# Kernel optimization log

Hardware: AMD Instinct MI355X
Metric: run time of the kernel (lower is better)

The kernel has to match this reference:

```python
import jax, jax.numpy as jnp
import numpy as np
import math

H, W = 32, 32
HID = 256
K = 4
B = 16
DIN = 272
DFF = 1024
L = 2
NB = 7
IMG_H, IMG_W = 256, 256
LN_EPS = 1e-5


def _layernorm(x, g, b):
    m = jnp.mean(x, axis=-1, keepdims=True)
    v = jnp.var(x, axis=-1, keepdims=True)
    return (x - m) / jnp.sqrt(v + LN_EPS) * g + b


def _neighbor_mask(h, w, nb):
    # (h*w, h*w): 0 inside the nb x nb window around each query pixel, -inf outside
    rr = jnp.repeat(jnp.arange(h), w)
    cc = jnp.tile(jnp.arange(w), h)
    near = (jnp.abs(rr[:, None] - rr[None, :]) <= nb // 2) & (
        jnp.abs(cc[:, None] - cc[None, :]) <= nb // 2
    )
    return jnp.where(near, 0.0, -jnp.inf).astype(jnp.float32)


def _pos_embed(row_embed, col_embed):
    # pos[i*w + j] = concat(col_embed[j], row_embed[i])  -> (h*w, hid)
    h, nf = row_embed.shape
    w = col_embed.shape[0]
    pe = jnp.concatenate(
        [
            jnp.broadcast_to(col_embed[None, :, :], (h, w, nf)),
            jnp.broadcast_to(row_embed[:, None, :], (h, w, nf)),
        ],
        axis=-1,
    )
    return pe.reshape(h * w, 2 * nf)


def _resize_bilinear_ac(x, oh, ow):
    # nn.UpsamplingBilinear2d => align_corners=True
    b, c, h, w = x.shape
    ys = jnp.arange(oh) * ((h - 1) / (oh - 1))
    y0 = jnp.floor(ys).astype(jnp.int32)
    y1 = jnp.minimum(y0 + 1, h - 1)
    fy = (ys - y0).astype(x.dtype)
    x = x[:, :, y0, :] * (1 - fy)[None, None, :, None] + x[:, :, y1, :] * fy[None, None, :, None]
    xs = jnp.arange(ow) * ((w - 1) / (ow - 1))
    x0 = jnp.floor(xs).astype(jnp.int32)
    x1 = jnp.minimum(x0 + 1, w - 1)
    fx = (xs - x0).astype(x.dtype)
    x = x[:, :, :, x0] * (1 - fx) + x[:, :, :, x1] * fx
    return x


def _forward(query_features, matched_features, qW, qb, kvW, kvb, row_embed, col_embed,
             aggW, aggb, n1g, n1b, l1W, l1b, l2W, l2b, n2g, n2b, outW, outb):
    b, c_in, h, w = query_features.shape
    n = h * w
    # b c h w -> b (h w) c, then input projections
    qt = query_features.transpose(0, 2, 3, 1).reshape(b, n, c_in) @ qW + qb  # (b,n,hid)
    kt = matched_features.transpose(0, 1, 3, 4, 2).reshape(K, b, n, c_in) @ kvW + kvb  # (K,b,n,hid)

    pos = _pos_embed(row_embed, col_embed)  # (n, hid); broadcast over batch
    mask = _neighbor_mask(h, w, NB)  # (n, n)
    scale = 1.0 / math.sqrt(qt.shape[-1])

    x = qt
    for l in range(L):
        qp = (x + pos) * scale            # q gets pos embed then scaled
        kp = kt + pos                     # k gets pos embed; v is the raw matched tokens
        scores = jnp.einsum('bnc,kbmc->kbnm', qp, kp) + mask
        attn = jax.nn.softmax(scores, axis=-1)
        o = jnp.einsum('kbnm,kbmc->bnkc', attn, kt).reshape(b, n, K * HID)
        o = o @ aggW[l] + aggb[l]
        x = _layernorm(x + o, n1g[l], n1b[l])
        ff = jax.nn.relu(x @ l1W[l] + l1b[l]) @ l2W[l] + l2b[l]
        x = _layernorm(x + ff, n2g[l], n2b[l])

    recon_tokens = x @ outW + outb  # (b,n,c_in)
    recon = recon_tokens.reshape(b, h, w, c_in).transpose(0, 3, 1, 2)
    pred = jnp.sqrt(jnp.sum((recon - query_features) ** 2, axis=1, keepdims=True))
    pred = (pred - pred.min()) / (pred.max() - pred.min())
    pred = _resize_bilinear_ac(pred, IMG_H, IMG_W)
    return recon, pred


def setup_inputs() -> dict:
    key = jax.random.key(0)
    ks = jax.random.split(key, 12)

    def nrm(k, shape, scale=0.02):
        return jax.random.normal(k, shape, jnp.float32) * scale

    return {
        'query_features': jax.random.normal(ks[0], (B, DIN, H, W), jnp.float32),
        'matched_features': jax.random.normal(ks[1], (K, B, DIN, H, W), jnp.float32),
        'qW': nrm(ks[2], (DIN, HID)), 'qb': jnp.zeros((HID,), jnp.float32),
        'kvW': nrm(ks[3], (DIN, HID)), 'kvb': jnp.zeros((HID,), jnp.float32),
        'row_embed': jax.random.uniform(ks[4], (H, HID // 2), jnp.float32),
        'col_embed': jax.random.uniform(ks[5], (W, HID // 2), jnp.float32),
        'aggW': nrm(ks[6], (L, K * HID, HID)), 'aggb': jnp.zeros((L, HID), jnp.float32),
        'n1g': jnp.ones((L, HID), jnp.float32), 'n1b': jnp.zeros((L, HID), jnp.float32),
        'l1W': nrm(ks[7], (L, HID, DFF)), 'l1b': jnp.zeros((L, DFF), jnp.float32),
        'l2W': nrm(ks[8], (L, DFF, HID)), 'l2b': jnp.zeros((L, HID), jnp.float32),
        'n2g': jnp.ones((L, HID), jnp.float32), 'n2b': jnp.zeros((L, HID), jnp.float32),
        'outW': nrm(ks[9], (HID, DIN)), 'outb': jnp.zeros((DIN,), jnp.float32),
    }


def reference(query_features, matched_features, qW, qb, kvW, kvb, row_embed, col_embed,
              aggW, aggb, n1g, n1b, l1W, l1b, l2W, l2b, n2g, n2b, outW, outb):
    return _forward(query_features, matched_features, qW, qb, kvW, kvb, row_embed,
                    col_embed, aggW, aggb, n1g, n1b, l1W, l1b, l2W, l2b, n2g, n2b,
                    outW, outb)
```

## Files before the change

### kernel.cpp

```cpp
#include <hip/hip_runtime.h>
#include <hip/hip_bf16.h>
#include <math.h>

#define BATCH 16
#define NTOK 1024
#define HID 256
#define KMEM 4
#define DIN 272
#define DINP 288
#define DFF 1024
#define LN_EPS 1e-5f

using short8 = __attribute__((ext_vector_type(8))) short;
using short4v = __attribute__((ext_vector_type(4))) short;
using floatx4 = __attribute__((ext_vector_type(4))) float;

__device__ inline short f2bf(float f) {
  unsigned u = __builtin_bit_cast(unsigned, f);
  u += 0x7fff + ((u >> 16) & 1);
  return (short)(u >> 16);
}
__device__ inline float bf2f(short s) {
  unsigned u = ((unsigned)(unsigned short)s) << 16;
  return __builtin_bit_cast(float, u);
}

__global__ __launch_bounds__(256) void pos_kernel(
    const float* __restrict__ row_e, const float* __restrict__ col_e,
    float* __restrict__ pos) {
  int t = blockIdx.x;
  int j = threadIdx.x;
  float v = (j < 128) ? col_e[(t & 31) * 128 + j]
                      : row_e[(t >> 5) * 128 + (j - 128)];
  pos[t * 256 + j] = v;
}

__global__ __launch_bounds__(256) void tcvt_kernel(
    const float* __restrict__ qf, const float* __restrict__ mf,
    short* __restrict__ qf_t, short* __restrict__ mf_t) {
  __shared__ short tile[32][33];
  int slice = blockIdx.x >> 5;
  int t0 = (blockIdx.x & 31) * 32;
  int c0 = blockIdx.y * 32;
  int tx = threadIdx.x & 31, ty = threadIdx.x >> 5;
  const float* s;
  short* d;
  if (slice < 16) {
    s = qf + (long)slice * DIN * NTOK;
    d = qf_t + (long)slice * NTOK * DINP;
  } else {
    s = mf + (long)(slice - 16) * DIN * NTOK;
    d = mf_t + (long)(slice - 16) * NTOK * DINP;
  }
#pragma unroll
  for (int i = 0; i < 4; i++) {
    int c = c0 + ty + i * 8;
    float v = (c < DIN) ? s[(long)c * NTOK + t0 + tx] : 0.f;
    tile[ty + i * 8][tx] = f2bf(v);
  }
  __syncthreads();
  d += (long)t0 * DINP + c0;
#pragma unroll
  for (int i = 0; i < 4; i++) {
    int tl = ty + i * 8;
    d[(long)tl * DINP + tx] = tile[tx][tl];
  }
}

struct WtJob {
  const float* src;
  short* dst;
  int K, Kd, N, ntx, start;
};
struct WtJobs {
  WtJob j[9];
};

__global__ __launch_bounds__(256) void wt_cvt_all_kernel(WtJobs jobs) {
  __shared__ short tile[32][33];
  int bid = blockIdx.x;
  int ji = 0;
#pragma unroll
  for (int i = 1; i < 9; ++i)
    if (bid >= jobs.j[i].start) ji = i;
  const float* W = jobs.j[ji].src;
  short* Wt = jobs.j[ji].dst;
  int K = jobs.j[ji].K, Kd = jobs.j[ji].Kd, N = jobs.j[ji].N;
  int local = bid - jobs.j[ji].start;
  int n0 = (local % jobs.j[ji].ntx) * 32;
  int k0 = (local / jobs.j[ji].ntx) * 32;
  int tx = threadIdx.x & 31, ty8 = threadIdx.x >> 5;
#pragma unroll
  for (int i = 0; i < 4; i++) {
    int k = k0 + ty8 + i * 8;
    int n = n0 + tx;
    float v = (k < K && n < N) ? W[(long)k * N + n] : 0.f;
    tile[ty8 + i * 8][tx] = f2bf(v);
  }
  __syncthreads();
#pragma unroll
  for (int i = 0; i < 4; i++) {
    int n = n0 + ty8 + i * 8;
    int k = k0 + tx;
    if (n < N && k < Kd) Wt[(long)n * Kd + k] = tile[tx][ty8 + i * 8];
  }
}

template <int OUTMODE>
__global__ __launch_bounds__(256) void gemm2_kernel(
    const short* __restrict__ A, const short* __restrict__ Wt,
    const float* __restrict__ bias, float* __restrict__ Cf,
    short* __restrict__ Cs, int M, int N, int K, int gxn,
    short* __restrict__ ktp, short* __restrict__ ktv,
    const float* __restrict__ pos, const float* __restrict__ qfp,
    float* __restrict__ ppart) {
  __shared__ short As[2][64][40];
  __shared__ short Bs[2][128][40];
  __shared__ float part_s[64][2];
  int nwg = gridDim.x;
  int cpx = nwg >> 3;
  int bid = blockIdx.x;
  int h = (bid & 7) * cpx + (bid >> 3);
  int cx = h % gxn;
  int ry = h / gxn;
  int row0 = ry * 64, col0 = cx * 128;
  int tid = threadIdx.x;
  int w = tid >> 6, lane = tid & 63;
  int wrow = (w >> 1) * 32, wcol = (w & 1) * 64;
  int lcol = lane & 15, kg = lane >> 4;

  int arow = tid >> 2, ak = (tid & 3) * 8;
  int brow = tid >> 2, bk = (tid & 3) * 8;
  const short* Ab = A + (long)row0 * K;
  const short* Bb = Wt + (long)col0 * K;
  bool bv0 = (col0 + brow) < N;
  bool bv1 = (col0 + brow + 64) < N;

  const short8 z8 = (short8){0, 0, 0, 0, 0, 0, 0, 0};
  short8 ra, rb0, rb1;
  ra = *reinterpret_cast<const short8*>(&Ab[(long)arow * K + ak]);
  rb0 = bv0 ? *reinterpret_cast<const short8*>(&Bb[(long)brow * K + bk]) : z8;
  rb1 = bv1 ? *reinterpret_cast<const short8*>(&Bb[(long)(brow + 64) * K + bk])
            : z8;
  *reinterpret_cast<short8*>(&As[0][arow][ak]) = ra;
  *reinterpret_cast<short8*>(&Bs[0][brow][bk]) = rb0;
  *reinterpret_cast<short8*>(&Bs[0][brow + 64][bk]) = rb1;
  __syncthreads();

  floatx4 acc[2][4];
#pragma unroll
  for (int m = 0; m < 2; ++m)
#pragma unroll
    for (int n = 0; n < 4; ++n) acc[m][n] = (floatx4){0.f, 0.f, 0.f, 0.f};

  int NT = K >> 5;
  for (int t = 0; t < NT; ++t) {
    int cur = t & 1;
    if (t + 1 < NT) {
      int ko = (t + 1) << 5;
      ra = *reinterpret_cast<const short8*>(&Ab[(long)arow * K + ko + ak]);
      rb0 = bv0 ? *reinterpret_cast<const short8*>(&Bb[(long)brow * K + ko + bk])
                : z8;
      rb1 = bv1 ? *reinterpret_cast<const short8*>(
                      &Bb[(long)(brow + 64) * K + ko + bk])
                : z8;
    }
    short8 af[2], bf[4];
#pragma unroll
    for (int m = 0; m < 2; ++m)
      af[m] = *reinterpret_cast<const short8*>(
          &As[cur][wrow + m * 16 + lcol][kg * 8]);
#pragma unroll
    for (int n = 0; n < 4; ++n)
      bf[n] = *reinterpret_cast<const short8*>(
          &Bs[cur][wcol + n * 16 + lcol][kg * 8]);
#pragma unroll
    for (int m = 0; m < 2; ++m)
#pragma unroll
      for (int n = 0; n < 4; ++n)
        acc[m][n] = __builtin_amdgcn_mfma_f32_16x16x32_bf16(af[m], bf[n],
                                                            acc[m][n], 0, 0, 0);
    if (t + 1 < NT) {
      int nxt = cur ^ 1;
      *reinterpret_cast<short8*>(&As[nxt][arow][ak]) = ra;
      *reinterpret_cast<short8*>(&Bs[nxt][brow][bk]) = rb0;
      *reinterpret_cast<short8*>(&Bs[nxt][brow + 64][bk]) = rb1;
    }
    __syncthreads();
  }

  if (OUTMODE == 4) {
    int bb = row0 >> 10;
    int tb0 = (row0 & 1023) + wrow;
    float sqp[2][4] = {};
#pragma unroll
    for (int n = 0; n < 4; ++n) {
      int c = col0 + wcol + n * 16 + lcol;
      if (c < N) {
        float bv = bias[c];
#pragma unroll
        for (int m = 0; m < 2; ++m) {
          int tb = tb0 + m * 16 + kg * 4;
          long addr = ((long)bb * DIN + c) * 1024 + tb;
          float4 qv = *reinterpret_cast<const float4*>(&qfp[addr]);
          float4 ov;
          float v0 = acc[m][n][0] + bv;
          float v1 = acc[m][n][1] + bv;
          float v2 = acc[m][n][2] + bv;
          float v3 = acc[m][n][3] + bv;
          ov.x = v0;
          ov.y = v1;
          ov.z = v2;
          ov.w = v3;
          float d0 = v0 - qv.x, d1 = v1 - qv.y, d2 = v2 - qv.z, d3 = v3 - qv.w;
          sqp[m][0] = fmaf(d0, d0, sqp[m][0]);
          sqp[m][1] = fmaf(d1, d1, sqp[m][1]);
          sqp[m][2] = fmaf(d2, d2, sqp[m][2]);
          sqp[m][3] = fmaf(d3, d3, sqp[m][3]);
          *reinterpret_cast<float4*>(&Cf[addr]) = ov;
        }
      }
    }
#pragma unroll
    for (int m = 0; m < 2; ++m)
#pragma unroll
      for (int q = 0; q < 4; ++q) {
        float s = sqp[m][q];
        s += __shfl_xor(s, 1);
        s += __shfl_xor(s, 2);
        s += __shfl_xor(s, 4);
        s += __shfl_xor(s, 8);
        if (lcol == 0) part_s[wrow + m * 16 + kg * 4 + q][w & 1] = s;
      }
    __syncthreads();
    if (tid < 64)
      ppart[(long)cx * 16384 + row0 + tid] = part_s[tid][0] + part_s[tid][1];
    return;
  }

#pragma unroll
  for (int n = 0; n < 4; ++n) {
    int c = col0 + wcol + n * 16 + lcol;
    if (c >= N) continue;
    float bv = bias[c];
#pragma unroll
    for (int m = 0; m < 2; ++m) {
      int rbase = row0 + wrow + m * 16 + kg * 4;
      if (OUTMODE == 0) {
#pragma unroll
        for (int q = 0; q < 4; ++q)
          Cf[(long)(rbase + q) * N + c] = acc[m][n][q] + bv;
      } else if (OUTMODE == 1) {
#pragma unroll
        for (int q = 0; q < 4; ++q)
          Cs[(long)(rbase + q) * N + c] = f2bf(fmaxf(acc[m][n][q] + bv, 0.f));
      } else if (OUTMODE == 3) {
#pragma unroll
        for (int q = 0; q < 4; ++q) {
          float val = acc[m][n][q] + bv;
          Cf[(long)(rbase + q) * N + c] = val;
          Cs[(long)(rbase + q) * N + c] = f2bf(val);
        }
      } else {
        int slice = rbase >> 10, tbase = rbase & 1023;
        short4v vt;
#pragma unroll
        for (int q = 0; q < 4; ++q) {
          float val = acc[m][n][q] + bv;
          vt[q] = f2bf(val);
          ktp[(long)(rbase + q) * 256 + c] =
              f2bf(val + pos[(tbase + q) * 256 + c]);
        }
        *reinterpret_cast<short4v*>(
            &ktv[(long)slice * (256 * 1024) + (long)c * 1024 + tbase]) = vt;
      }
    }
  }
}

__global__ __launch_bounds__(256) void gemm_ln_kernel(
    const short* __restrict__ A, const short* __restrict__ Wt,
    const float* __restrict__ bias, const float* __restrict__ res,
    const float* __restrict__ g, const float* __restrict__ bta,
    float* __restrict__ xout, short* __restrict__ x16out, int K) {
  __shared__ short As[2][32][40];
  __shared__ short Bs[2][256][40];
  __shared__ float st_s[32][4];
  __shared__ float st_s2[32][4];
  int tid = threadIdx.x;
  int row0 = blockIdx.x * 32;
  int w = tid >> 6, lane = tid & 63, lcol = lane & 15, kg = lane >> 4;
  int arow = tid >> 2, ak = (tid & 3) * 8;
  int brow = tid >> 2, bk = (tid & 3) * 8;
  const short* Ab = A + (long)row0 * K;

  short8 ra, rb[4];
  if (tid < 128) ra = *reinterpret_cast<const short8*>(&Ab[(long)arow * K + ak]);
#pragma unroll
  for (int i = 0; i < 4; ++i)
    rb[i] = *reinterpret_cast<const short8*>(&Wt[(long)(brow + i * 64) * K + bk]);
  if (tid < 128) *reinterpret_cast<short8*>(&As[0][arow][ak]) = ra;
#pragma unroll
  for (int i = 0; i < 4; ++i)
    *reinterpret_cast<short8*>(&Bs[0][brow + i * 64][bk]) = rb[i];
  __syncthreads();

  floatx4 acc[2][4];
#pragma unroll
  for (int m = 0; m < 2; ++m)
#pragma unroll
    for (int n = 0; n < 4; ++n) acc[m][n] = (floatx4){0.f, 0.f, 0.f, 0.f};

  int NT = K >> 5;
  for (int t = 0; t < NT; ++t) {
    int cur = t & 1;
    if (t + 1 < NT) {
      int ko = (t + 1) << 5;
      if (tid < 128)
        ra = *reinterpret_cast<const short8*>(&Ab[(long)arow * K + ko + ak]);
#pragma unroll
      for (int i = 0; i < 4; ++i)
        rb[i] = *reinterpret_cast<const short8*>(
            &Wt[(long)(brow + i * 64) * K + ko + bk]);
    }
    short8 af[2], bf[4];
#pragma unroll
    for (int m = 0; m < 2; ++m)
      af[m] =
          *reinterpret_cast<const short8*>(&As[cur][m * 16 + lcol][kg * 8]);
#pragma unroll
    for (int n = 0; n < 4; ++n)
      bf[n] = *reinterpret_cast<const short8*>(
          &Bs[cur][w * 64 + n * 16 + lcol][kg * 8]);
#pragma unroll
    for (int m = 0; m < 2; ++m)
#pragma unroll
      for (int n = 0; n < 4; ++n)
        acc[m][n] = __builtin_amdgcn_mfma_f32_16x16x32_bf16(af[m], bf[n],
                                                            acc[m][n], 0, 0, 0);
    if (t + 1 < NT) {
      int nxt = cur ^ 1;
      if (tid < 128) *reinterpret_cast<short8*>(&As[nxt][arow][ak]) = ra;
#pragma unroll
      for (int i = 0; i < 4; ++i)
        *reinterpret_cast<short8*>(&Bs[nxt][brow + i * 64][bk]) = rb[i];
    }
    __syncthreads();
  }

  float val[2][4][4];
#pragma unroll
  for (int n = 0; n < 4; ++n) {
    int c = w * 64 + n * 16 + lcol;
    float bv = bias[c];
#pragma unroll
    for (int m = 0; m < 2; ++m) {
      int rbase = row0 + m * 16 + kg * 4;
#pragma unroll
      for (int q = 0; q < 4; ++q)
        val[m][n][q] = acc[m][n][q] + bv + res[(long)(rbase + q) * 256 + c];
    }
  }
  float s[2][4], s2[2][4];
#pragma unroll
  for (int m = 0; m < 2; ++m)
#pragma unroll
    for (int q = 0; q < 4; ++q) {
      float ss = 0.f, ss2 = 0.f;
#pragma unroll
      for (int n = 0; n < 4; ++n) {
        float v = val[m][n][q];
        ss += v;
        ss2 = fmaf(v, v, ss2);
      }
      ss += __shfl_xor(ss, 1);
      ss2 += __shfl_xor(ss2, 1);
      ss += __shfl_xor(ss, 2);
      ss2 += __shfl_xor(ss2, 2);
      ss += __shfl_xor(ss, 4);
      ss2 += __shfl_xor(ss2, 4);
      ss += __shfl_xor(ss, 8);
      ss2 += __shfl_xor(ss2, 8);
      s[m][q] = ss;
      s2[m][q] = ss2;
    }
  if (lcol == 0) {
#pragma unroll
    for (int m = 0; m < 2; ++m)
#pragma unroll
      for (int q = 0; q < 4; ++q) {
        st_s[m * 16 + kg * 4 + q][w] = s[m][q];
        st_s2[m * 16 + kg * 4 + q][w] = s2[m][q];
      }
  }
  __syncthreads();
#pragma unroll
  for (int m = 0; m < 2; ++m)
#pragma unroll
    for (int q = 0; q < 4; ++q) {
      int row = m * 16 + kg * 4 + q;
      float4 a4 = *reinterpret_cast<const float4*>(&st_s[row][0]);
      float4 b4 = *reinterpret_cast<const float4*>(&st_s2[row][0]);
      float S = (a4.x + a4.y) + (a4.z + a4.w);
      float S2 = (b4.x + b4.y) + (b4.z + b4.w);
      float mean = S * (1.f / 256.f);
      float var = S2 * (1.f / 256.f) - mean * mean;
      float inv = rsqrtf(var + LN_EPS);
#pragma unroll
      for (int n = 0; n < 4; ++n) {
        int c = w * 64 + n * 16 + lcol;
        float o = (val[m][n][q] - mean) * inv * g[c] + bta[c];
        long addr = (long)(row0 + row) * 256 + c;
        xout[addr] = o;
        x16out[addr] = f2bf(o);
      }
    }
}

__global__ __launch_bounds__(256) void attn_kernel(
    const short* __restrict__ x16, const short* __restrict__ ktp,
    const short* __restrict__ ktv, const float* __restrict__ pos,
    short* __restrict__ o) {
  __shared__ short QP_s[32][264];
  __shared__ float st_mx[32][4];
  __shared__ float st_sm[32][4];
  int h = blockIdx.x;
  int xcd = h & 7, jj = h >> 3;
  int sidx = xcd * 8 + (jj >> 5);
  int r = jj & 31;
  int b = sidx & 15, k = sidx >> 4;
  int tid = threadIdx.x;
  int w = tid >> 6, lane = tid & 63, lcol = lane & 15, kg = lane >> 4;
  const float scale = 0.0625f;

  const short* xb = x16 + ((long)b * NTOK + r * 32) * HID;
  const float* pq = pos + (long)r * 32 * HID;
#pragma unroll
  for (int p = 0; p < 4; ++p) {
    int f = p * 256 + tid;
    int row = f >> 5, c8 = (f & 31) << 3;
    short8 xv = *reinterpret_cast<const short8*>(&xb[row * HID + c8]);
    float4 p0 = *reinterpret_cast<const float4*>(&pq[row * HID + c8]);
    float4 p1 = *reinterpret_cast<const float4*>(&pq[row * HID + c8 + 4]);
    short8 s;
    s[0] = f2bf((bf2f(xv[0]) + p0.x) * scale);
    s[1] = f2bf((bf2f(xv[1]) + p0.y) * scale);
    s[2] = f2bf((bf2f(xv[2]) + p0.z) * scale);
    s[3] = f2bf((bf2f(xv[3]) + p0.w) * scale);
    s[4] = f2bf((bf2f(xv[4]) + p1.x) * scale);
    s[5] = f2bf((bf2f(xv[5]) + p1.y) * scale);
    s[6] = f2bf((bf2f(xv[6]) + p1.z) * scale);
    s[7] = f2bf((bf2f(xv[7]) + p1.w) * scale);
    *reinterpret_cast<short8*>(&QP_s[row][c8]) = s;
  }
  __syncthreads();

  int r0 = max(r - 3, 0), r1 = min(r + 3, 31);
  int nkr = r1 - r0 + 1, nm = nkr * 32;
  const short* ktpb = ktp + ((long)(k * BATCH + b)) * NTOK * HID;
  const short* ktvb = ktv + ((long)(k * BATCH + b)) * NTOK * HID;

  floatx4 acc[2][4];
#pragma unroll
  for (int m = 0; m < 2; ++m)
#pragma unroll
    for (int n = 0; n < 4; ++n) acc[m][n] = (floatx4){0.f, 0.f, 0.f, 0.f};

  int tokn[4];
#pragma unroll
  for (int n = 0; n < 4; ++n) {
    int nf = w * 4 + n;
    int krow = min(r0 + (nf >> 1), 31);
    tokn[n] = krow * 32 + ((nf & 1) << 4) + lcol;
  }
#pragma unroll
  for (int s = 0; s < 8; ++s) {
    short8 af0 = *reinterpret_cast<const short8*>(&QP_s[lcol][s * 32 + kg * 8]);
    short8 af1 =
        *reinterpret_cast<const short8*>(&QP_s[16 + lcol][s * 32 + kg * 8]);
#pragma unroll
    for (int n = 0; n < 4; ++n) {
      short8 bfr = *reinterpret_cast<const short8*>(
          &ktpb[(long)tokn[n] * HID + s * 32 + kg * 8]);
      acc[0][n] =
          __builtin_amdgcn_mfma_f32_16x16x32_bf16(af0, bfr, acc[0][n], 0, 0, 0);
      acc[1][n] =
          __builtin_amdgcn_mfma_f32_16x16x32_bf16(af1, bfr, acc[1][n], 0, 0, 0);
    }
  }

  const float NEG = -3.0e38f;
  float mx[2][4];
#pragma unroll
  for (int m = 0; m < 2; ++m)
#pragma unroll
    for (int q = 0; q < 4; ++q) {
      int rr = m * 16 + kg * 4 + q;
      float vmax = NEG;
#pragma unroll
      for (int n = 0; n < 4; ++n) {
        int col = (w * 4 + n) * 16 + lcol;
        int ck = col & 31;
        bool ok = (col < nm) && (ck - rr <= 3) && (rr - ck <= 3);
        float v = ok ? acc[m][n][q] : NEG;
        acc[m][n][q] = v;
        vmax = fmaxf(vmax, v);
      }
      vmax = fmaxf(vmax, __shfl_xor(vmax, 1));
      vmax = fmaxf(vmax, __shfl_xor(vmax, 2));
      vmax = fmaxf(vmax, __shfl_xor(vmax, 4));
      vmax = fmaxf(vmax, __shfl_xor(vmax, 8));
      mx[m][q] = vmax;
    }
  if (lcol == 0) {
#pragma unroll
    for (int m = 0; m < 2; ++m)
#pragma unroll
      for (int q = 0; q < 4; ++q) st_mx[m * 16 + kg * 4 + q][w] = mx[m][q];
  }
  __syncthreads();
  float sm[2][4];
#pragma unroll
  for (int m = 0; m < 2; ++m)
#pragma unroll
    for (int q = 0; q < 4; ++q) {
      int rr = m * 16 + kg * 4 + q;
      float4 v4 = *reinterpret_cast<const float4*>(&st_mx[rr][0]);
      float g = fmaxf(fmaxf(v4.x, v4.y), fmaxf(v4.z, v4.w));
      float ss = 0.f;
#pragma unroll
      for (int n = 0; n < 4; ++n) {
        float v = acc[m][n][q];
        float pv = (v > -1.0e30f) ? exp2f((v - g) * 1.4426950408889634f) : 0.f;
        acc[m][n][q] = pv;
        ss += pv;
      }
      ss += __shfl_xor(ss, 1);
      ss += __shfl_xor(ss, 2);
      ss += __shfl_xor(ss, 4);
      ss += __shfl_xor(ss, 8);
      sm[m][q] = ss;
    }
  if (lcol == 0) {
#pragma unroll
    for (int m = 0; m < 2; ++m)
#pragma unroll
      for (int q = 0; q < 4; ++q) st_sm[m * 16 + kg * 4 + q][w] = sm[m][q];
  }
  __syncthreads();
#pragma unroll
  for (int m = 0; m < 2; ++m)
#pragma unroll
    for (int q = 0; q < 4; ++q) {
      int rr = m * 16 + kg * 4 + q;
      float4 v4 = *reinterpret_cast<const float4*>(&st_sm[rr][0]);
      float rinv = 1.0f / (v4.x + v4.y + v4.z + v4.w);
#pragma unroll
      for (int n = 0; n < 4; ++n) {
        QP_s[rr][(w * 4 + n) * 16 + lcol] = f2bf(acc[m][n][q] * rinv);
      }
    }
  __syncthreads();

  floatx4 oacc[2][4];
#pragma unroll
  for (int m = 0; m < 2; ++m)
#pragma unroll
    for (int n = 0; n < 4; ++n) oacc[m][n] = (floatx4){0.f, 0.f, 0.f, 0.f};

  for (int kb = 0; kb < nkr; ++kb) {
    short8 ap0 = *reinterpret_cast<const short8*>(&QP_s[lcol][kb * 32 + kg * 8]);
    short8 ap1 =
        *reinterpret_cast<const short8*>(&QP_s[16 + lcol][kb * 32 + kg * 8]);
    int tokb = (r0 + kb) * 32;
#pragma unroll
    for (int n = 0; n < 4; ++n) {
      int ch = w * 64 + n * 16 + lcol;
      short8 bv = *reinterpret_cast<const short8*>(
          &ktvb[(long)ch * NTOK + tokb + kg * 8]);
      oacc[0][n] =
          __builtin_amdgcn_mfma_f32_16x16x32_bf16(ap0, bv, oacc[0][n], 0, 0, 0);
      oacc[1][n] =
          __builtin_amdgcn_mfma_f32_16x16x32_bf16(ap1, bv, oacc[1][n], 0, 0, 0);
    }
  }
#pragma unroll
  for (int m = 0; m < 2; ++m)
#pragma unroll
    for (int n = 0; n < 4; ++n) {
      int ch = w * 64 + n * 16 + lcol;
#pragma unroll
      for (int q = 0; q < 4; ++q) {
        int rr = m * 16 + kg * 4 + q;
        o[((long)b * NTOK + r * 32 + rr) * (KMEM * HID) + k * HID + ch] =
            f2bf(oacc[m][n][q]);
      }
    }
}

__global__ __launch_bounds__(256) void minmax_kernel(
    const float* __restrict__ ppart, float* __restrict__ pred_sq,
    float* __restrict__ mnmx) {
  int tid = threadIdx.x;
  float mn = INFINITY, mx = -INFINITY;
  for (int i = tid; i < BATCH * NTOK; i += 256) {
    float v = ppart[i] + ppart[16384 + i] + ppart[32768 + i];
    pred_sq[i] = v;
    float sv = sqrtf(v);
    mn = fminf(mn, sv);
    mx = fmaxf(mx, sv);
  }
#pragma unroll
  for (int off = 32; off > 0; off >>= 1) {
    mn = fminf(mn, __shfl_xor(mn, off));
    mx = fmaxf(mx, __shfl_xor(mx, off));
  }
  __shared__ float smn[4], smx[4];
  int wave = tid >> 6, lane = tid & 63;
  if (lane == 0) {
    smn[wave] = mn;
    smx[wave] = mx;
  }
  __syncthreads();
  if (tid == 0) {
    mn = fminf(fminf(smn[0], smn[1]), fminf(smn[2], smn[3]));
    mx = fmaxf(fmaxf(smx[0], smx[1]), fmaxf(smx[2], smx[3]));
    mnmx[0] = mn;
    mnmx[1] = mx;
  }
}

__global__ __launch_bounds__(256) void resize_kernel(
    const float* __restrict__ pred_sq, const float* __restrict__ mnmx,
    float* __restrict__ out) {
  long idx = (long)blockIdx.x * 256 + threadIdx.x;
  if (idx >= (long)BATCH * 256 * 256) return;
  int b = (int)(idx >> 16);
  int oy = (int)((idx >> 8) & 255), ox = (int)(idx & 255);
  float mn = mnmx[0], mx = mnmx[1];
  float inv = 1.0f / (mx - mn);
  float ys = oy * (31.0f / 255.0f);
  int y0 = (int)floorf(ys);
  int y1 = min(y0 + 1, 31);
  float fy = ys - (float)y0;
  float xs = ox * (31.0f / 255.0f);
  int x0 = (int)floorf(xs);
  int x1 = min(x0 + 1, 31);
  float fx = xs - (float)x0;
  const float* p = pred_sq + b * NTOK;
  float v00 = sqrtf(p[y0 * 32 + x0]), v01 = sqrtf(p[y0 * 32 + x1]);
  float v10 = sqrtf(p[y1 * 32 + x0]), v11 = sqrtf(p[y1 * 32 + x1]);
  float cA = v00 * (1.f - fy) + v10 * fy;
  float cB = v01 * (1.f - fy) + v11 * fy;
  float v = cA * (1.f - fx) + cB * fx;
  out[idx] = (v - mn) * inv;
}

extern "C" void kernel_launch(void* const* d_in, const int* in_sizes, int n_in,
                              void* d_out, int out_size, void* d_ws,
                              size_t ws_size, hipStream_t stream) {
  const float* qf = (const float*)d_in[0];
  const float* mf = (const float*)d_in[1];
  const float* qW = (const float*)d_in[2];
  const float* qb = (const float*)d_in[3];
  const float* kvW = (const float*)d_in[4];
  const float* kvb = (const float*)d_in[5];
  const float* row_e = (const float*)d_in[6];
  const float* col_e = (const float*)d_in[7];
  const float* aggW = (const float*)d_in[8];
  const float* aggb = (const float*)d_in[9];
  const float* n1g = (const float*)d_in[10];
  const float* n1b = (const float*)d_in[11];
  const float* l1W = (const float*)d_in[12];
  const float* l1b = (const float*)d_in[13];
  const float* l2W = (const float*)d_in[14];
  const float* l2b = (const float*)d_in[15];
  const float* n2g = (const float*)d_in[16];
  const float* n2b = (const float*)d_in[17];
  const float* outW = (const float*)d_in[18];
  const float* outb = (const float*)d_in[19];

  float* out = (float*)d_out;
  float* recon = out;
  float* pred = out + (long)BATCH * DIN * NTOK;

  float* ws = (float*)d_ws;
  float* pos = ws;
  float* x = pos + 262144;
  short* x16 = (short*)(x + 4194304);
  short* ktp = x16 + 4194304;
  short* ktv = ktp + 16777216;
  short* buf16 = ktv + 16777216;
  float* tmp256 = (float*)(buf16 + 16777216);
  short* wt = (short*)(tmp256 + 4194304);
  short* wt_agg0 = wt;
  short* wt_agg1 = wt_agg0 + 262144;
  short* wt_l1_0 = wt_agg1 + 262144;
  short* wt_l1_1 = wt_l1_0 + 262144;
  short* wt_l2_0 = wt_l1_1 + 262144;
  short* wt_l2_1 = wt_l2_0 + 262144;
  short* wt_out = wt_l2_1 + 262144;
  short* wt_q = wt_out + 69632;
  short* wt_kv = wt_q + 73728;
  float* pred_part = (float*)(wt_kv + 73728);
  float* pred_sq = pred_part + 49152;
  float* mnmx = pred_sq + 16384;
  short* qf_t = ktp;
  short* mf_t = buf16;

  pos_kernel<<<NTOK, 256, 0, stream>>>(row_e, col_e, pos);

  {
    WtJobs jobs;
    jobs.j[0] = {aggW, wt_agg0, 1024, 1024, 256, 8, 0};
    jobs.j[1] = {aggW + 262144, wt_agg1, 1024, 1024, 256, 8, 256};
    jobs.j[2] = {l1W, wt_l1_0, 256, 256, 1024, 32, 512};
    jobs.j[3] = {l1W + 262144, wt_l1_1, 256, 256, 1024, 32, 768};
    jobs.j[4] = {l2W, wt_l2_0, 1024, 1024, 256, 8, 1024};
    jobs.j[5] = {l2W + 262144, wt_l2_1, 1024, 1024, 256, 8, 1280};
    jobs.j[6] = {outW, wt_out, 256, 256, 272, 9, 1536};
    jobs.j[7] = {qW, wt_q, 272, 288, 256, 8, 1608};
    jobs.j[8] = {kvW, wt_kv, 272, 288, 256, 8, 1680};
    wt_cvt_all_kernel<<<1752, 256, 0, stream>>>(jobs);
  }

  tcvt_kernel<<<dim3(2560, 9), 256, 0, stream>>>(qf, mf, qf_t, mf_t);

  gemm2_kernel<3><<<512, 256, 0, stream>>>(
      qf_t, wt_q, qb, x, x16, BATCH * NTOK, HID, DINP, 2, nullptr, nullptr,
      nullptr, nullptr, nullptr);
  gemm2_kernel<2><<<2048, 256, 0, stream>>>(
      mf_t, wt_kv, kvb, nullptr, nullptr, KMEM * BATCH * NTOK, HID, DINP, 2,
      ktp, ktv, pos, nullptr, nullptr);

  for (int l = 0; l < 2; l++) {
    attn_kernel<<<2048, 256, 0, stream>>>(x16, ktp, ktv, pos, buf16);
    gemm_ln_kernel<<<512, 256, 0, stream>>>(
        buf16, l ? wt_agg1 : wt_agg0, aggb + l * 256, x, n1g + l * 256,
        n1b + l * 256, x, x16, KMEM * HID);
    gemm2_kernel<1><<<2048, 256, 0, stream>>>(
        x16, l ? wt_l1_1 : wt_l1_0, l1b + l * 1024, nullptr, buf16,
        BATCH * NTOK, DFF, HID, 8, nullptr, nullptr, nullptr, nullptr,
        nullptr);
    gemm_ln_kernel<<<512, 256, 0, stream>>>(
        buf16, l ? wt_l2_1 : wt_l2_0, l2b + l * 256, x, n2g + l * 256,
        n2b + l * 256, x, x16, DFF);
  }

  gemm2_kernel<4><<<768, 256, 0, stream>>>(
      x16, wt_out, outb, recon, nullptr, BATCH * NTOK, DIN, HID, 3, nullptr,
      nullptr, nullptr, qf, pred_part);
  minmax_kernel<<<1, 256, 0, stream>>>(pred_part, pred_sq, mnmx);
  resize_kernel<<<(BATCH * 256 * 256) / 256, 256, 0, stream>>>(pred_sq, mnmx,
                                                               pred);
}
```

Measured before the change: 420.7 us.

## Precompute scaled query-plus-pos bf16 once per layer in producer epilogues

Moves the (x + pos) * scale bf16 query construction out of the attention kernel into the epilogues of the query-projection GEMM and the layer-0 FFN LayerNorm kernel, which now write a separate q16 buffer. Attention reads query fragments directly from global memory instead of staging them through shared memory, dropping one barrier and the per-block pos reads. Each query tile was previously rebuilt by every block sharing it (across all K memory slices), so this removes redundant conversion work. It also skips the fp32 x write in the final LayerNorm, whose output is never read again. The cost is an extra q16 buffer write and uncached global reads of A fragments inside the MFMA loop.

```diff
diff --git a/kernel.cpp b/kernel.cpp
--- a/kernel.cpp
+++ b/kernel.cpp
@@ -24,6 +24,8 @@
   unsigned u = ((unsigned)(unsigned short)s) << 16;
   return __builtin_bit_cast(float, u);
 }
+
+#define QSCALE 0.0625f
 
 __global__ __launch_bounds__(256) void pos_kernel(
     const float* __restrict__ row_e, const float* __restrict__ col_e,
@@ -259,7 +261,8 @@
         for (int q = 0; q < 4; ++q) {
           float val = acc[m][n][q] + bv;
           Cf[(long)(rbase + q) * N + c] = val;
-          Cs[(long)(rbase + q) * N + c] = f2bf(val);
+          Cs[(long)(rbase + q) * N + c] =
+              f2bf((val + pos[((rbase + q) & 1023) * 256 + c]) * QSCALE);
         }
       } else {
         int slice = rbase >> 10, tbase = rbase & 1023;
@@ -278,11 +281,13 @@
   }
 }
 
+template <bool EX, bool EQ>
 __global__ __launch_bounds__(256) void gemm_ln_kernel(
     const short* __restrict__ A, const short* __restrict__ Wt,
     const float* __restrict__ bias, const float* __restrict__ res,
     const float* __restrict__ g, const float* __restrict__ bta,
-    float* __restrict__ xout, short* __restrict__ x16out, int K) {
+    float* __restrict__ xout, short* __restrict__ x16out,
+    const float* __restrict__ pos, short* __restrict__ q16out, int K) {
   __shared__ short As[2][32][40];
   __shared__ short Bs[2][256][40];
   __shared__ float st_s[32][4];
@@ -411,17 +416,19 @@
         int c = w * 64 + n * 16 + lcol;
         float o = (val[m][n][q] - mean) * inv * g[c] + bta[c];
         long addr = (long)(row0 + row) * 256 + c;
-        xout[addr] = o;
+        if (EX) xout[addr] = o;
         x16out[addr] = f2bf(o);
+        if (EQ)
+          q16out[addr] =
+              f2bf((o + pos[((row0 + row) & 1023) * 256 + c]) * QSCALE);
       }
     }
 }
 
 __global__ __launch_bounds__(256) void attn_kernel(
-    const short* __restrict__ x16, const short* __restrict__ ktp,
-    const short* __restrict__ ktv, const float* __restrict__ pos,
-    short* __restrict__ o) {
-  __shared__ short QP_s[32][264];
+    const short* __restrict__ q16, const short* __restrict__ ktp,
+    const short* __restrict__ ktv, short* __restrict__ o) {
+  __shared__ short P_s[32][264];
   __shared__ float st_mx[32][4];
   __shared__ float st_sm[32][4];
   int h = blockIdx.x;
@@ -431,32 +438,10 @@
   int b = sidx & 15, k = sidx >> 4;
   int tid = threadIdx.x;
   int w = tid >> 6, lane = tid & 63, lcol = lane & 15, kg = lane >> 4;
-  const float scale = 0.0625f;
-
-  const short* xb = x16 + ((long)b * NTOK + r * 32) * HID;
-  const float* pq = pos + (long)r * 32 * HID;
-#pragma unroll
-  for (int p = 0; p < 4; ++p) {
-    int f = p * 256 + tid;
-    int row = f >> 5, c8 = (f & 31) << 3;
-    short8 xv = *reinterpret_cast<const short8*>(&xb[row * HID + c8]);
-    float4 p0 = *reinterpret_cast<const float4*>(&pq[row * HID + c8]);
-    float4 p1 = *reinterpret_cast<const float4*>(&pq[row * HID + c8 + 4]);
-    short8 s;
-    s[0] = f2bf((bf2f(xv[0]) + p0.x) * scale);
-    s[1] = f2bf((bf2f(xv[1]) + p0.y) * scale);
-    s[2] = f2bf((bf2f(xv[2]) + p0.z) * scale);
-    s[3] = f2bf((bf2f(xv[3]) + p0.w) * scale);
-    s[4] = f2bf((bf2f(xv[4]) + p1.x) * scale);
-    s[5] = f2bf((bf2f(xv[5]) + p1.y) * scale);
-    s[6] = f2bf((bf2f(xv[6]) + p1.z) * scale);
-    s[7] = f2bf((bf2f(xv[7]) + p1.w) * scale);
-    *reinterpret_cast<short8*>(&QP_s[row][c8]) = s;
-  }
-  __syncthreads();
 
   int r0 = max(r - 3, 0), r1 = min(r + 3, 31);
   int nkr = r1 - r0 + 1, nm = nkr * 32;
+  const short* qb = q16 + ((long)b * NTOK + r * 32) * HID;
   const short* ktpb = ktp + ((long)(k * BATCH + b)) * NTOK * HID;
   const short* ktvb = ktv + ((long)(k * BATCH + b)) * NTOK * HID;
 
@@ -475,9 +460,10 @@
   }
 #pragma unroll
   for (int s = 0; s < 8; ++s) {
-    short8 af0 = *reinterpret_cast<const short8*>(&QP_s[lcol][s * 32 + kg * 8]);
-    short8 af1 =
-        *reinterpret_cast<const short8*>(&QP_s[16 + lcol][s * 32 + kg * 8]);
+    short8 af0 = *reinterpret_cast<const short8*>(
+        &qb[(long)lcol * HID + s * 32 + kg * 8]);
+    short8 af1 = *reinterpret_cast<const short8*>(
+        &qb[(long)(16 + lcol) * HID + s * 32 + kg * 8]);
 #pragma unroll
     for (int n = 0; n < 4; ++n) {
       short8 bfr = *reinterpret_cast<const short8*>(
@@ -557,7 +543,7 @@
       float rinv = 1.0f / (v4.x + v4.y + v4.z + v4.w);
 #pragma unroll
       for (int n = 0; n < 4; ++n) {
-        QP_s[rr][(w * 4 + n) * 16 + lcol] = f2bf(acc[m][n][q] * rinv);
+        P_s[rr][(w * 4 + n) * 16 + lcol] = f2bf(acc[m][n][q] * rinv);
       }
     }
   __syncthreads();
@@ -569,9 +555,9 @@
     for (int n = 0; n < 4; ++n) oacc[m][n] = (floatx4){0.f, 0.f, 0.f, 0.f};
 
   for (int kb = 0; kb < nkr; ++kb) {
-    short8 ap0 = *reinterpret_cast<const short8*>(&QP_s[lcol][kb * 32 + kg * 8]);
+    short8 ap0 = *reinterpret_cast<const short8*>(&P_s[lcol][kb * 32 + kg * 8]);
     short8 ap1 =
-        *reinterpret_cast<const short8*>(&QP_s[16 + lcol][kb * 32 + kg * 8]);
+        *reinterpret_cast<const short8*>(&P_s[16 + lcol][kb * 32 + kg * 8]);
     int tokb = (r0 + kb) * 32;
 #pragma unroll
     for (int n = 0; n < 4; ++n) {
@@ -688,7 +674,8 @@
   float* pos = ws;
   float* x = pos + 262144;
   short* x16 = (short*)(x + 4194304);
-  short* ktp = x16 + 4194304;
+  short* q16 = x16 + 4194304;
+  short* ktp = q16 + 4194304;
   short* ktv = ktp + 16777216;
   short* buf16 = ktv + 16777216;
   float* tmp256 = (float*)(buf16 + 16777216);
@@ -727,24 +714,29 @@
   tcvt_kernel<<<dim3(2560, 9), 256, 0, stream>>>(qf, mf, qf_t, mf_t);
 
   gemm2_kernel<3><<<512, 256, 0, stream>>>(
-      qf_t, wt_q, qb, x, x16, BATCH * NTOK, HID, DINP, 2, nullptr, nullptr,
-      nullptr, nullptr, nullptr);
+      qf_t, wt_q, qb, x, q16, BATCH * NTOK, HID, DINP, 2, nullptr, nullptr,
+      pos, nullptr, nullptr);
   gemm2_kernel<2><<<2048, 256, 0, stream>>>(
       mf_t, wt_kv, kvb, nullptr, nullptr, KMEM * BATCH * NTOK, HID, DINP, 2,
       ktp, ktv, pos, nullptr, nullptr);
 
   for (int l = 0; l < 2; l++) {
-    attn_kernel<<<2048, 256, 0, stream>>>(x16, ktp, ktv, pos, buf16);
-    gemm_ln_kernel<<<512, 256, 0, stream>>>(
+    attn_kernel<<<2048, 256, 0, stream>>>(q16, ktp, ktv, buf16);
+    gemm_ln_kernel<true, false><<<512, 256, 0, stream>>>(
         buf16, l ? wt_agg1 : wt_agg0, aggb + l * 256, x, n1g + l * 256,
-        n1b + l * 256, x, x16, KMEM * HID);
+        n1b + l * 256, x, x16, nullptr, nullptr, KMEM * HID);
     gemm2_kernel<1><<<2048, 256, 0, stream>>>(
         x16, l ? wt_l1_1 : wt_l1_0, l1b + l * 1024, nullptr, buf16,
         BATCH * NTOK, DFF, HID, 8, nullptr, nullptr, nullptr, nullptr,
         nullptr);
-    gemm_ln_kernel<<<512, 256, 0, stream>>>(
-        buf16, l ? wt_l2_1 : wt_l2_0, l2b + l * 256, x, n2g + l * 256,
-        n2b + l * 256, x, x16, DFF);
+    if (l == 0) {
+      gemm_ln_kernel<true, true><<<512, 256, 0, stream>>>(
+          buf16, wt_l2_0, l2b, x, n2g, n2b, x, x16, pos, q16, DFF);
+    } else {
+      gemm_ln_kernel<false, false><<<512, 256, 0, stream>>>(
+          buf16, wt_l2_1, l2b + 256, x, n2g + 256, n2b + 256, x, x16, nullptr,
+          nullptr, DFF);
+    }
   }
 
   gemm2_kernel<4><<<768, 256, 0, stream>>>(
```

Measured after the change: 447.3 us. 6.3% more time.
